# Optimization experiments

Hardware: AMD Instinct MI355X
Metric: run time of the kernel (lower is better)

## Reference

```python
import jax, jax.numpy as jnp
import numpy as np

DRUG_DIM, TARGET_DIM, HEADS, DIM_HEAD = 768, 2560, 8, 96
INNER = HEADS * DIM_HEAD
NEG = -1000000.0
LN_EPS = 1e-5


def setup_inputs() -> dict:
    key = jax.random.key(0)
    ks = jax.random.split(key, 10)
    b, n, m = 16, 256, 1024
    drug = jax.random.normal(ks[0], (b, n, DRUG_DIM), dtype=jnp.float32)
    target = jax.random.normal(ks[1], (b, m, TARGET_DIM), dtype=jnp.float32)
    drug_mask = jax.random.randint(ks[2], (b, n), 0, 2, dtype=jnp.int32)
    pro_mask = jax.random.randint(ks[3], (b, m), 0, 2, dtype=jnp.int32)
    # parameters (torch Linear weight is (out,in); store as (in,out) for x @ W)
    Wq = jax.random.normal(ks[4], (DRUG_DIM, INNER), dtype=jnp.float32) / np.sqrt(DRUG_DIM)
    Wk = jax.random.normal(ks[5], (TARGET_DIM, INNER), dtype=jnp.float32) / np.sqrt(TARGET_DIM)
    Wv = jax.random.normal(ks[6], (TARGET_DIM, INNER), dtype=jnp.float32) / np.sqrt(TARGET_DIM)
    Wo = jax.random.normal(ks[7], (INNER, DRUG_DIM), dtype=jnp.float32) / np.sqrt(INNER)
    bo = jnp.zeros((DRUG_DIM,), dtype=jnp.float32)
    gamma = jnp.ones((DRUG_DIM,), dtype=jnp.float32)
    beta = jnp.zeros((DRUG_DIM,), dtype=jnp.float32)
    return {"drug": drug, "target": target, "drug_mask": drug_mask,
            "pro_mask": pro_mask, "Wq": Wq, "Wk": Wk, "Wv": Wv,
            "Wo": Wo, "bo": bo, "gamma": gamma, "beta": beta}


def reference(drug, target, drug_mask, pro_mask, Wq, Wk, Wv, Wo, bo, gamma, beta):
    b, n, _ = drug.shape
    m = target.shape[1]
    scale = DIM_HEAD ** -0.5
    # projections -> (b, h, len, d)
    q = (drug @ Wq).reshape(b, n, HEADS, DIM_HEAD).transpose(0, 2, 1, 3)
    k = (target @ Wk).reshape(b, m, HEADS, DIM_HEAD).transpose(0, 2, 1, 3)
    v = (target @ Wv).reshape(b, m, HEADS, DIM_HEAD).transpose(0, 2, 1, 3)
    dots = jnp.einsum('bhnd,bhmd->bhnm', q, k) * scale
    # dual mask: positions where drug_mask==0 (rows) OR pro_mask==0 (cols) -> -1e6
    valid = (drug_mask[:, None, :, None] != 0) & (pro_mask[:, None, None, :] != 0)
    masked_dots = jnp.where(valid, dots, NEG)
    attn = jax.nn.softmax(masked_dots, axis=-1)
    out = jnp.einsum('bhnm,bhmd->bhnd', attn, v)
    out = out.transpose(0, 2, 1, 3).reshape(b, n, INNER)
    out = out @ Wo + bo
    # residual + LayerNorm
    x = out + drug
    mu = jnp.mean(x, axis=-1, keepdims=True)
    var = jnp.mean(jnp.square(x - mu), axis=-1, keepdims=True)
    out = (x - mu) * jax.lax.rsqrt(var + LN_EPS) * gamma + beta
    return (out, attn)
```

## Files before the change

kernel.cpp:

```cpp
#include <hip/hip_runtime.h>

typedef short s16x8 __attribute__((ext_vector_type(8)));
typedef float f32x4 __attribute__((ext_vector_type(4)));

__device__ __forceinline__ unsigned short f2bf(float f) {
    unsigned int u = __builtin_bit_cast(unsigned int, f);
    unsigned int r = u + 0x7FFFu + ((u >> 16) & 1u);
    return (unsigned short)(r >> 16);
}

__device__ __forceinline__ void gload16(const unsigned short* g, unsigned short* l) {
    __builtin_amdgcn_global_load_lds(
        (const __attribute__((address_space(1))) unsigned int*)g,
        (__attribute__((address_space(3))) unsigned int*)l, 16, 0, 0);
}

__device__ __forceinline__ s16x8 ldf(const unsigned short* p) {
    return *reinterpret_cast<const s16x8*>(p);
}

__global__ __launch_bounds__(256) void cvt_bf16_2(
    const float* __restrict__ in0, unsigned short* __restrict__ out0, int n0blk, int n0,
    const float* __restrict__ in1, unsigned short* __restrict__ out1, int n1) {
    const float* in;
    unsigned short* out;
    int n, bid;
    if (blockIdx.x < n0blk) { in = in0; out = out0; n = n0; bid = blockIdx.x; }
    else { in = in1; out = out1; n = n1; bid = blockIdx.x - n0blk; }
    int nblk = (blockIdx.x < n0blk) ? n0blk : (gridDim.x - n0blk);
    int i = (bid * 256 + threadIdx.x) * 8;
    int stride = nblk * 256 * 8;
    for (; i < n; i += stride) {
        float4 a = *reinterpret_cast<const float4*>(in + i);
        float4 b = *reinterpret_cast<const float4*>(in + i + 4);
        uint4 o;
        o.x = (unsigned int)f2bf(a.x) | ((unsigned int)f2bf(a.y) << 16);
        o.y = (unsigned int)f2bf(a.z) | ((unsigned int)f2bf(a.w) << 16);
        o.z = (unsigned int)f2bf(b.x) | ((unsigned int)f2bf(b.y) << 16);
        o.w = (unsigned int)f2bf(b.z) | ((unsigned int)f2bf(b.w) << 16);
        *reinterpret_cast<uint4*>(out + i) = o;
    }
}

__global__ __launch_bounds__(256) void transpose2_bf16(
    const float* __restrict__ W0, const float* __restrict__ W1,
    unsigned short* __restrict__ T0, unsigned short* __restrict__ T1, int K, int N) {
    __shared__ float t[32][33];
    const float* W = blockIdx.z ? W1 : W0;
    unsigned short* Wt = blockIdx.z ? T1 : T0;
    int k0 = blockIdx.x * 32, n0 = blockIdx.y * 32;
    int tid = threadIdx.x;
    int r = tid >> 5, c = tid & 31;
    for (int p = 0; p < 4; ++p)
        t[p * 8 + r][c] = W[(size_t)(k0 + p * 8 + r) * N + n0 + c];
    __syncthreads();
    for (int p = 0; p < 4; ++p)
        Wt[(size_t)(n0 + p * 8 + r) * K + k0 + c] = f2bf(t[c][p * 8 + r]);
}

template <int OUTMODE>
__global__ __launch_bounds__(256, 2) void gemm_db(
    const unsigned short* __restrict__ A, const unsigned short* __restrict__ Bt,
    int M, int N, int K,
    float* __restrict__ Cf,
    unsigned short* __restrict__ outA, unsigned short* __restrict__ outVt,
    int seqlen) {
    extern __shared__ __align__(16) unsigned short smem[];
    unsigned short* As = smem;
    unsigned short* Bs = smem + 16384;

    int tid = threadIdx.x, wid = tid >> 6, lane = tid & 63;
    int nb = N / 128;
    int nwg = gridDim.x, bid = blockIdx.x;
    int wg = (bid & 7) * (nwg >> 3) + (bid >> 3);
    int tm = wg / nb, tn = wg % nb;
    int m0 = tm * 128, n0 = tn * 128;
    int wm = (wid >> 1) * 64, wn = (wid & 1) * 64;
    int lrow = lane & 15, lkc = lane >> 4;

    int lrsub = lane >> 3;
    int gch = (lane & 7) ^ lrsub;
    const unsigned short* gA[4];
    const unsigned short* gB[4];
    unsigned short* lA[4];
    unsigned short* lB[4];
#pragma unroll
    for (int p = 0; p < 4; ++p) {
        int r = (wid * 4 + p) * 8 + lrsub;
        gA[p] = A + (size_t)(m0 + r) * K + gch * 8;
        gB[p] = Bt + (size_t)(n0 + r) * K + gch * 8;
        lA[p] = As + (wid * 4 + p) * 512;
        lB[p] = Bs + (wid * 4 + p) * 512;
    }

    int offA[2][4], offB[2][4];
#pragma unroll
    for (int kh = 0; kh < 2; ++kh)
#pragma unroll
        for (int i = 0; i < 4; ++i) {
            int ra = wm + i * 16 + lrow;
            offA[kh][i] = ra * 64 + (((kh * 4 + lkc) ^ (ra & 7)) * 8);
            int rb = wn + i * 16 + lrow;
            offB[kh][i] = rb * 64 + (((kh * 4 + lkc) ^ (rb & 7)) * 8);
        }

    int NT = K / 64;
    f32x4 acc[4][4] = {};

#pragma unroll
    for (int p = 0; p < 4; ++p) { gload16(gA[p], lA[p]); gload16(gB[p], lB[p]); }

    int cur = 0;
    for (int t = 0; t < NT; ++t) {
        __syncthreads();
        if (t + 1 < NT) {
            int nxt = (cur ^ 1) * 8192;
            int koff = (t + 1) * 64;
#pragma unroll
            for (int p = 0; p < 4; ++p) {
                gload16(gA[p] + koff, lA[p] + nxt);
                gload16(gB[p] + koff, lB[p] + nxt);
            }
        }
        const unsigned short* Ab = As + cur * 8192;
        const unsigned short* Bb = Bs + cur * 8192;
#pragma unroll
        for (int kh = 0; kh < 2; ++kh) {
            s16x8 af[4], bfv[4];
#pragma unroll
            for (int i = 0; i < 4; ++i) af[i] = ldf(&Ab[offA[kh][i]]);
#pragma unroll
            for (int j = 0; j < 4; ++j) bfv[j] = ldf(&Bb[offB[kh][j]]);
#pragma unroll
            for (int i = 0; i < 4; ++i)
#pragma unroll
                for (int j = 0; j < 4; ++j)
                    acc[i][j] = __builtin_amdgcn_mfma_f32_16x16x32_bf16(af[i], bfv[j], acc[i][j], 0, 0, 0);
        }
        cur ^= 1;
    }

    int orow4 = (lane >> 4) * 4;
    int bblk = (OUTMODE == 1) ? (m0 / seqlen) : 0;
    for (int i = 0; i < 4; ++i)
        for (int j = 0; j < 4; ++j)
            for (int r = 0; r < 4; ++r) {
                int row = m0 + wm + i * 16 + orow4 + r;
                int col = n0 + wn + j * 16 + lrow;
                float v = acc[i][j][r];
                if constexpr (OUTMODE == 0) {
                    Cf[(size_t)row * N + col] = v;
                } else {
                    int s = row - bblk * seqlen;
                    unsigned short hv = f2bf(v);
                    if (col < 768) {
                        int h = col / 96, d = col - h * 96;
                        outA[(((size_t)(bblk * 8 + h)) * seqlen + s) * 96 + d] = hv;
                    } else {
                        int cc = col - 768;
                        int h = cc / 96, d = cc - h * 96;
                        outVt[(((size_t)(bblk * 8 + h)) * 96 + d) * seqlen + s] = hv;
                    }
                }
            }
}

#define MT 64
__global__ __launch_bounds__(256) void attn_kernel(
    const unsigned short* __restrict__ Qb,
    const unsigned short* __restrict__ Kb,
    const unsigned short* __restrict__ Vt,
    const int* __restrict__ drug_mask,
    const int* __restrict__ pro_mask,
    float* __restrict__ attn_out,
    unsigned short* __restrict__ AO)
{
    constexpr float scale = 0.10206207261596575f;
    __shared__ __align__(16) unsigned short Qs[64][104];
    __shared__ __align__(16) unsigned short Ks[MT][104];
    __shared__ __align__(16) unsigned short Vts[96][MT + 8];
    __shared__ __align__(16) unsigned short Ps[4][16][MT + 8];
    __shared__ float colv[1024];

    int tid = threadIdx.x, wid = tid >> 6, lane = tid & 63;
    int bh = blockIdx.x, nt = blockIdx.y;
    int b = bh >> 3, h = bh & 7;
    const unsigned short* Qg = Qb + (size_t)bh * 256 * 96 + (size_t)nt * 64 * 96;
    const unsigned short* Kg = Kb + (size_t)bh * 1024 * 96;
    const unsigned short* Vg = Vt + (size_t)bh * 96 * 1024;

    for (int idx = tid; idx < 64 * 12; idx += 256) {
        int r = idx / 12, s = idx % 12;
        *reinterpret_cast<uint4*>(&Qs[r][s * 8]) =
            *reinterpret_cast<const uint4*>(&Qg[r * 96 + s * 8]);
    }
    for (int m = tid; m < 1024; m += 256)
        colv[m] = (pro_mask[b * 1024 + m] != 0) ? 1.0f : 0.0f;

    int lrow = lane & 15, lkg = lane >> 4;
    int qrow0 = nt * 64 + wid * 16;
    float rv[4];
    for (int r = 0; r < 4; ++r)
        rv[r] = (drug_mask[b * 256 + qrow0 + lkg * 4 + r] != 0) ? 1.0f : 0.0f;

    __syncthreads();
    s16x8 qa[3];
    for (int kk = 0; kk < 3; ++kk)
        qa[kk] = ldf(&Qs[wid * 16 + lrow][kk * 32 + lkg * 8]);

    float mrun[4], srun[4];
    for (int r = 0; r < 4; ++r) { mrun[r] = -3.0e38f; srun[r] = 0.f; }

    for (int mt = 0; mt < 1024; mt += MT) {
        __syncthreads();
        for (int idx = tid; idx < MT * 12; idx += 256) {
            int r = idx / 12, s = idx % 12;
            *reinterpret_cast<uint4*>(&Ks[r][s * 8]) =
                *reinterpret_cast<const uint4*>(&Kg[(size_t)(mt + r) * 96 + s * 8]);
        }
        __syncthreads();
        float sv[MT / 16][4];
        for (int nf = 0; nf < MT / 16; ++nf) {
            f32x4 acc = {};
            for (int kk = 0; kk < 3; ++kk) {
                s16x8 bb = ldf(&Ks[nf * 16 + lrow][kk * 32 + lkg * 8]);
                acc = __builtin_amdgcn_mfma_f32_16x16x32_bf16(qa[kk], bb, acc, 0, 0, 0);
            }
            float cv = colv[mt + nf * 16 + lrow];
            for (int r = 0; r < 4; ++r)
                sv[nf][r] = (rv[r] * cv != 0.f) ? acc[r] * scale : -1.0e6f;
        }
        for (int r = 0; r < 4; ++r) {
            float v = sv[0][r];
            for (int nf = 1; nf < MT / 16; ++nf) v = fmaxf(v, sv[nf][r]);
            for (int o = 1; o < 16; o <<= 1) v = fmaxf(v, __shfl_xor(v, o));
            float nm = fmaxf(mrun[r], v);
            float ts = 0.f;
            for (int nf = 0; nf < MT / 16; ++nf) ts += __expf(sv[nf][r] - nm);
            for (int o = 1; o < 16; o <<= 1) ts += __shfl_xor(ts, o);
            srun[r] = srun[r] * __expf(mrun[r] - nm) + ts;
            mrun[r] = nm;
        }
    }
    float sinv[4];
    for (int r = 0; r < 4; ++r) sinv[r] = 1.0f / srun[r];

    f32x4 oacc[6] = {};
    for (int mt = 0; mt < 1024; mt += MT) {
        __syncthreads();
        for (int idx = tid; idx < MT * 12; idx += 256) {
            int r = idx / 12, s = idx % 12;
            *reinterpret_cast<uint4*>(&Ks[r][s * 8]) =
                *reinterpret_cast<const uint4*>(&Kg[(size_t)(mt + r) * 96 + s * 8]);
        }
        for (int idx = tid; idx < 96 * (MT / 8); idx += 256) {
            int r = idx / (MT / 8), s = idx % (MT / 8);
            *reinterpret_cast<uint4*>(&Vts[r][s * 8]) =
                *reinterpret_cast<const uint4*>(&Vg[(size_t)r * 1024 + mt + s * 8]);
        }
        __syncthreads();
        for (int nf = 0; nf < MT / 16; ++nf) {
            f32x4 acc = {};
            for (int kk = 0; kk < 3; ++kk) {
                s16x8 bb = ldf(&Ks[nf * 16 + lrow][kk * 32 + lkg * 8]);
                acc = __builtin_amdgcn_mfma_f32_16x16x32_bf16(qa[kk], bb, acc, 0, 0, 0);
            }
            float cv = colv[mt + nf * 16 + lrow];
            for (int r = 0; r < 4; ++r) {
                float sel = (rv[r] * cv != 0.f) ? acc[r] * scale : -1.0e6f;
                float p = __expf(sel - mrun[r]) * sinv[r];
                attn_out[((size_t)bh * 256 + qrow0 + lkg * 4 + r) * 1024 + mt + nf * 16 + lrow] = p;
                Ps[wid][lkg * 4 + r][nf * 16 + lrow] = f2bf(p);
            }
        }
        __syncthreads();
        for (int kk = 0; kk < MT / 32; ++kk) {
            s16x8 pa = ldf(&Ps[wid][lrow][kk * 32 + lkg * 8]);
            for (int df = 0; df < 6; ++df) {
                s16x8 vb = ldf(&Vts[df * 16 + lrow][kk * 32 + lkg * 8]);
                oacc[df] = __builtin_amdgcn_mfma_f32_16x16x32_bf16(pa, vb, oacc[df], 0, 0, 0);
            }
        }
    }
    for (int df = 0; df < 6; ++df)
        for (int r = 0; r < 4; ++r) {
            int grow = b * 256 + qrow0 + lkg * 4 + r;
            int gcol = h * 96 + df * 16 + lrow;
            AO[(size_t)grow * 768 + gcol] = f2bf(oacc[df][r]);
        }
}

__global__ __launch_bounds__(256) void ln_kernel(
    const float* __restrict__ O, const float* __restrict__ drug,
    const float* __restrict__ bo, const float* __restrict__ gamma,
    const float* __restrict__ beta, float* __restrict__ out) {
    int row = blockIdx.x, tid = threadIdx.x;
    __shared__ float red[4];
    float x[3], s = 0.f;
    for (int i = 0; i < 3; ++i) {
        int j = tid + i * 256;
        x[i] = O[(size_t)row * 768 + j] + bo[j] + drug[(size_t)row * 768 + j];
        s += x[i];
    }
    for (int o = 32; o; o >>= 1) s += __shfl_xor(s, o);
    if ((tid & 63) == 0) red[tid >> 6] = s;
    __syncthreads();
    float mu = (red[0] + red[1] + red[2] + red[3]) * (1.0f / 768.0f);
    float v = 0.f;
    for (int i = 0; i < 3; ++i) { float d = x[i] - mu; v += d * d; }
    for (int o = 32; o; o >>= 1) v += __shfl_xor(v, o);
    __syncthreads();
    if ((tid & 63) == 0) red[tid >> 6] = v;
    __syncthreads();
    float var = (red[0] + red[1] + red[2] + red[3]) * (1.0f / 768.0f);
    float rs = rsqrtf(var + 1e-5f);
    for (int i = 0; i < 3; ++i) {
        int j = tid + i * 256;
        out[(size_t)row * 768 + j] = (x[i] - mu) * rs * gamma[j] + beta[j];
    }
}

extern "C" void kernel_launch(void* const* d_in, const int* in_sizes, int n_in,
                              void* d_out, int out_size, void* d_ws, size_t ws_size,
                              hipStream_t stream) {
    const float* drug   = (const float*)d_in[0];
    const float* target = (const float*)d_in[1];
    const int*   dmask  = (const int*)d_in[2];
    const int*   pmask  = (const int*)d_in[3];
    const float* Wq = (const float*)d_in[4];
    const float* Wk = (const float*)d_in[5];
    const float* Wv = (const float*)d_in[6];
    const float* Wo = (const float*)d_in[7];
    const float* bo = (const float*)d_in[8];
    const float* gm = (const float*)d_in[9];
    const float* bt = (const float*)d_in[10];

    char* w = (char*)d_ws;
    unsigned short* Wtq  = (unsigned short*)(w + 0);
    unsigned short* Wtkv = (unsigned short*)(w + 1179648);
    unsigned short* Wto  = (unsigned short*)(w + 9043968);
    unsigned short* Qb   = (unsigned short*)(w + 10223616);
    unsigned short* Kb   = (unsigned short*)(w + 16515072);
    unsigned short* Vtb  = (unsigned short*)(w + 41680896);
    unsigned short* AO   = (unsigned short*)(w + 66846720);
    float*          Otmp = (float*)(w + 73138176);
    unsigned short* drugb = (unsigned short*)(w + 85721088);

    float* out_ln   = (float*)d_out;
    float* attn_out = (float*)d_out + 3145728;
    unsigned short* targetb = (unsigned short*)attn_out;

    cvt_bf16_2<<<2560, 256, 0, stream>>>(target, targetb, 2048, 41943040,
                                         drug, drugb, 3145728);

    transpose2_bf16<<<dim3(24, 24, 2), 256, 0, stream>>>(Wq, Wo, Wtq, Wto, 768, 768);
    transpose2_bf16<<<dim3(80, 24, 2), 256, 0, stream>>>(
        Wk, Wv, Wtkv, Wtkv + (size_t)768 * 2560, 2560, 768);

    gemm_db<1><<<1536, 256, 65536, stream>>>(targetb, Wtkv, 16384, 1536, 2560,
                                             nullptr, Kb, Vtb, 1024);
    gemm_db<1><<<192, 256, 65536, stream>>>(drugb, Wtq, 4096, 768, 768,
                                            nullptr, Qb, nullptr, 256);
    attn_kernel<<<dim3(128, 4), 256, 0, stream>>>(Qb, Kb, Vtb, dmask, pmask, attn_out, AO);
    gemm_db<0><<<192, 256, 65536, stream>>>(AO, Wto, 4096, 768, 768,
                                            Otmp, nullptr, nullptr, 256);
    ln_kernel<<<4096, 256, 0, stream>>>(Otmp, drug, bo, gm, bt, out_ln);
}
```

Baseline: 335.7 us.

## Register-prefetch K/V tiles and vectorize attention-probability stores via LDS

K and V tiles for the next iteration are loaded into registers while the current tile is computed, so the global-load latency overlaps with MFMA work. The scattered per-element fp32 attention writes are replaced by float4 stores read back from the bf16 P tile in LDS, which coalesces the large attn output. A block-wide barrier is swapped for a wave-local lgkmcnt wait. The attn output now carries bf16 precision instead of fp32, which adds rounding error.

```diff
diff --git a/kernel.cpp b/kernel.cpp
--- a/kernel.cpp
+++ b/kernel.cpp
@@ -7,6 +7,10 @@
     unsigned int u = __builtin_bit_cast(unsigned int, f);
     unsigned int r = u + 0x7FFFu + ((u >> 16) & 1u);
     return (unsigned short)(r >> 16);
+}
+
+__device__ __forceinline__ float bf2f(unsigned short h) {
+    return __builtin_bit_cast(float, ((unsigned int)h) << 16);
 }
 
 __device__ __forceinline__ void gload16(const unsigned short* g, unsigned short* l) {
@@ -203,6 +207,14 @@
     for (int r = 0; r < 4; ++r)
         rv[r] = (drug_mask[b * 256 + qrow0 + lkg * 4 + r] != 0) ? 1.0f : 0.0f;
 
+    int kr[3], kc[3], vr[3], vc[3];
+#pragma unroll
+    for (int p = 0; p < 3; ++p) {
+        int idx = tid + p * 256;
+        kr[p] = idx / 12; kc[p] = (idx % 12) * 8;
+        vr[p] = idx / 8;  vc[p] = (idx % 8) * 8;
+    }
+
     __syncthreads();
     s16x8 qa[3];
     for (int kk = 0; kk < 3; ++kk)
@@ -211,31 +223,47 @@
     float mrun[4], srun[4];
     for (int r = 0; r < 4; ++r) { mrun[r] = -3.0e38f; srun[r] = 0.f; }
 
-    for (int mt = 0; mt < 1024; mt += MT) {
+    uint4 kreg[3];
+#pragma unroll
+    for (int p = 0; p < 3; ++p)
+        kreg[p] = *reinterpret_cast<const uint4*>(&Kg[(size_t)kr[p] * 96 + kc[p]]);
+
+    for (int tno = 0; tno < 16; ++tno) {
         __syncthreads();
-        for (int idx = tid; idx < MT * 12; idx += 256) {
-            int r = idx / 12, s = idx % 12;
-            *reinterpret_cast<uint4*>(&Ks[r][s * 8]) =
-                *reinterpret_cast<const uint4*>(&Kg[(size_t)(mt + r) * 96 + s * 8]);
+#pragma unroll
+        for (int p = 0; p < 3; ++p)
+            *reinterpret_cast<uint4*>(&Ks[kr[p]][kc[p]]) = kreg[p];
+        if (tno < 15) {
+            const unsigned short* Kn = Kg + (size_t)(tno + 1) * 64 * 96;
+#pragma unroll
+            for (int p = 0; p < 3; ++p)
+                kreg[p] = *reinterpret_cast<const uint4*>(&Kn[(size_t)kr[p] * 96 + kc[p]]);
         }
         __syncthreads();
+        int mt = tno * MT;
         float sv[MT / 16][4];
+#pragma unroll
         for (int nf = 0; nf < MT / 16; ++nf) {
             f32x4 acc = {};
+#pragma unroll
             for (int kk = 0; kk < 3; ++kk) {
                 s16x8 bb = ldf(&Ks[nf * 16 + lrow][kk * 32 + lkg * 8]);
                 acc = __builtin_amdgcn_mfma_f32_16x16x32_bf16(qa[kk], bb, acc, 0, 0, 0);
             }
             float cv = colv[mt + nf * 16 + lrow];
+#pragma unroll
             for (int r = 0; r < 4; ++r)
                 sv[nf][r] = (rv[r] * cv != 0.f) ? acc[r] * scale : -1.0e6f;
         }
+#pragma unroll
         for (int r = 0; r < 4; ++r) {
             float v = sv[0][r];
+#pragma unroll
             for (int nf = 1; nf < MT / 16; ++nf) v = fmaxf(v, sv[nf][r]);
             for (int o = 1; o < 16; o <<= 1) v = fmaxf(v, __shfl_xor(v, o));
             float nm = fmaxf(mrun[r], v);
             float ts = 0.f;
+#pragma unroll
             for (int nf = 0; nf < MT / 16; ++nf) ts += __expf(sv[nf][r] - nm);
             for (int o = 1; o < 16; o <<= 1) ts += __shfl_xor(ts, o);
             srun[r] = srun[r] * __expf(mrun[r] - nm) + ts;
@@ -245,41 +273,77 @@
     float sinv[4];
     for (int r = 0; r < 4; ++r) sinv[r] = 1.0f / srun[r];
 
+    uint4 vreg[3];
+#pragma unroll
+    for (int p = 0; p < 3; ++p) {
+        kreg[p] = *reinterpret_cast<const uint4*>(&Kg[(size_t)kr[p] * 96 + kc[p]]);
+        vreg[p] = *reinterpret_cast<const uint4*>(&Vg[(size_t)vr[p] * 1024 + vc[p]]);
+    }
+
     f32x4 oacc[6] = {};
-    for (int mt = 0; mt < 1024; mt += MT) {
+    for (int tno = 0; tno < 16; ++tno) {
+        int mt = tno * MT;
         __syncthreads();
-        for (int idx = tid; idx < MT * 12; idx += 256) {
-            int r = idx / 12, s = idx % 12;
-            *reinterpret_cast<uint4*>(&Ks[r][s * 8]) =
-                *reinterpret_cast<const uint4*>(&Kg[(size_t)(mt + r) * 96 + s * 8]);
-        }
-        for (int idx = tid; idx < 96 * (MT / 8); idx += 256) {
-            int r = idx / (MT / 8), s = idx % (MT / 8);
-            *reinterpret_cast<uint4*>(&Vts[r][s * 8]) =
-                *reinterpret_cast<const uint4*>(&Vg[(size_t)r * 1024 + mt + s * 8]);
+#pragma unroll
+        for (int p = 0; p < 3; ++p) {
+            *reinterpret_cast<uint4*>(&Ks[kr[p]][kc[p]]) = kreg[p];
+            *reinterpret_cast<uint4*>(&Vts[vr[p]][vc[p]]) = vreg[p];
+        }
+        if (tno < 15) {
+            const unsigned short* Kn = Kg + (size_t)(tno + 1) * 64 * 96;
+            int mn = mt + MT;
+#pragma unroll
+            for (int p = 0; p < 3; ++p) {
+                kreg[p] = *reinterpret_cast<const uint4*>(&Kn[(size_t)kr[p] * 96 + kc[p]]);
+                vreg[p] = *reinterpret_cast<const uint4*>(&Vg[(size_t)vr[p] * 1024 + mn + vc[p]]);
+            }
         }
         __syncthreads();
+#pragma unroll
         for (int nf = 0; nf < MT / 16; ++nf) {
             f32x4 acc = {};
+#pragma unroll
             for (int kk = 0; kk < 3; ++kk) {
                 s16x8 bb = ldf(&Ks[nf * 16 + lrow][kk * 32 + lkg * 8]);
                 acc = __builtin_amdgcn_mfma_f32_16x16x32_bf16(qa[kk], bb, acc, 0, 0, 0);
             }
             float cv = colv[mt + nf * 16 + lrow];
+#pragma unroll
             for (int r = 0; r < 4; ++r) {
                 float sel = (rv[r] * cv != 0.f) ? acc[r] * scale : -1.0e6f;
                 float p = __expf(sel - mrun[r]) * sinv[r];
-                attn_out[((size_t)bh * 256 + qrow0 + lkg * 4 + r) * 1024 + mt + nf * 16 + lrow] = p;
                 Ps[wid][lkg * 4 + r][nf * 16 + lrow] = f2bf(p);
             }
         }
-        __syncthreads();
+        asm volatile("s_waitcnt lgkmcnt(0)" ::: "memory");
+        __builtin_amdgcn_sched_barrier(0);
+#pragma unroll
         for (int kk = 0; kk < MT / 32; ++kk) {
             s16x8 pa = ldf(&Ps[wid][lrow][kk * 32 + lkg * 8]);
+#pragma unroll
             for (int df = 0; df < 6; ++df) {
                 s16x8 vb = ldf(&Vts[df * 16 + lrow][kk * 32 + lkg * 8]);
                 oacc[df] = __builtin_amdgcn_mfma_f32_16x16x32_bf16(pa, vb, oacc[df], 0, 0, 0);
             }
+        }
+        {
+            int r16 = lane >> 2, cb = (lane & 3) * 16;
+            s16x8 pA = ldf(&Ps[wid][r16][cb]);
+            s16x8 pB = ldf(&Ps[wid][r16][cb + 8]);
+            float* dst = &attn_out[((size_t)bh * 256 + qrow0 + r16) * 1024 + mt + cb];
+            float4 o0, o1, o2, o3;
+            o0.x = bf2f((unsigned short)pA[0]); o0.y = bf2f((unsigned short)pA[1]);
+            o0.z = bf2f((unsigned short)pA[2]); o0.w = bf2f((unsigned short)pA[3]);
+            o1.x = bf2f((unsigned short)pA[4]); o1.y = bf2f((unsigned short)pA[5]);
+            o1.z = bf2f((unsigned short)pA[6]); o1.w = bf2f((unsigned short)pA[7]);
+            o2.x = bf2f((unsigned short)pB[0]); o2.y = bf2f((unsigned short)pB[1]);
+            o2.z = bf2f((unsigned short)pB[2]); o2.w = bf2f((unsigned short)pB[3]);
+            o3.x = bf2f((unsigned short)pB[4]); o3.y = bf2f((unsigned short)pB[5]);
+            o3.z = bf2f((unsigned short)pB[6]); o3.w = bf2f((unsigned short)pB[7]);
+            reinterpret_cast<float4*>(dst)[0] = o0;
+            reinterpret_cast<float4*>(dst)[1] = o1;
+            reinterpret_cast<float4*>(dst)[2] = o2;
+            reinterpret_cast<float4*>(dst)[3] = o3;
         }
     }
     for (int df = 0; df < 6; ++df)
```

Measured after the change: 374.4 us. 1.12x slower.
